# Kernel tuning notes

Measured on AMD Instinct MI355X. Metric: run time of the kernel, lower is better.

Reference implementation:

```python
import jax, jax.numpy as jnp
import numpy as np

HEAD_DIM = 128


def block_causal_mask(cu_seqlens, seq_len, dtype):
    # positions -> which packed document each token belongs to
    positions = jnp.arange(seq_len)
    seq_ids = jnp.searchsorted(cu_seqlens, positions, side='right') - 1
    same_seq = seq_ids[:, None] == seq_ids[None, :]
    causal = positions[None, :] <= positions[:, None]  # key_pos <= query_pos
    neg_inf = jnp.asarray(float('-inf'), dtype)
    return jnp.where(same_seq & causal, jnp.asarray(0.0, dtype), neg_inf)


def setup_inputs() -> dict:
    key = jax.random.key(0)
    kq, kk, kv = jax.random.split(key, 3)
    B, H, S, D = 1, 8, 4096, HEAD_DIM
    q = jax.random.normal(kq, (B, H, S, D), dtype=jnp.float32)
    k = jax.random.normal(kk, (B, H, S, D), dtype=jnp.float32)
    v = jax.random.normal(kv, (B, H, S, D), dtype=jnp.float32)
    # 4 packed documents of length 1024 each; cu_seqlens[-1] == seq_len
    cu_seqlens = jnp.array([0, 1024, 2048, 3072, 4096], dtype=jnp.int32)
    return {"q": q, "k": k, "v": v, "cu_seqlens": cu_seqlens, "max_seqlen": 1024}


def reference(q, k, v, cu_seqlens, max_seqlen):
    seq_len = q.shape[2]
    scale = 1.0 / jnp.sqrt(jnp.asarray(q.shape[-1], q.dtype))
    mask = block_causal_mask(cu_seqlens, seq_len, q.dtype)  # [S, S]
    # scores: [B, H, Sq, Sk]
    scores = jnp.einsum('bhqd,bhkd->bhqk', q, k) * scale + mask
    probs = jax.nn.softmax(scores, axis=-1)
    return jnp.einsum('bhqk,bhkd->bhqd', probs, v)
```

## Files before the change

### kernel.cpp

```cpp
#include <hip/hip_runtime.h>
#include <hip/hip_bf16.h>


#define HD 128
#define BR 64
#define BC 64

typedef __attribute__((ext_vector_type(8))) short short8;
typedef __attribute__((ext_vector_type(4))) float floatx4;

__device__ inline unsigned packbf2(float lo, float hi) {
    __hip_bfloat162 h2 = __float22bfloat162_rn(make_float2(lo, hi));
    return *reinterpret_cast<unsigned*>(&h2);
}
__device__ inline short bfs(float f) {
    __hip_bfloat16 b = __float2bfloat16(f);
    return *reinterpret_cast<short*>(&b);
}

__device__ inline void gll16(const void* g, void* l) {
    __builtin_amdgcn_global_load_lds(
        (const __attribute__((address_space(1))) unsigned int*)g,
        (__attribute__((address_space(3))) unsigned int*)l, 16, 0, 0);
}

__global__ __launch_bounds__(256) void prepack(
    const float* __restrict__ K, const float* __restrict__ V,
    unsigned short* __restrict__ wsK, unsigned short* __restrict__ wsVT,
    int S)
{
    const int tid = threadIdx.x;
    const int nKblk = (8 * S * 16) / 256;
    const int bid = blockIdx.x;
    if (bid < nKblk) {
        const int cid = bid * 256 + tid;
        const int row = cid >> 4;
        const int c   = cid & 15;
        const float* src = K + (size_t)row * HD + c * 8;
        float4 f0 = *(const float4*)src;
        float4 f1 = *(const float4*)(src + 4);
        union { uint4 q; unsigned u[4]; } w;
        w.u[0] = packbf2(f0.x, f0.y); w.u[1] = packbf2(f0.z, f0.w);
        w.u[2] = packbf2(f1.x, f1.y); w.u[3] = packbf2(f1.z, f1.w);
        *(uint4*)((char*)wsK + (size_t)row * 256 + ((c * 16) ^ ((row & 7) << 4))) = w.q;
    } else {
        const int ntile = S >> 6;
        const int b = bid - nKblk;
        const int h = b / ntile;
        const int t = b - h * ntile;
        const int d  = tid & 127;
        const int jj = tid >> 7;
        const float* vb = V + ((size_t)h * S + t * 64) * HD + d;
        char* dstrow = (char*)wsVT + ((size_t)(h * ntile + t) * HD + d) * 128;
        const int dx = (d & 7) << 4;
        #pragma unroll
        for (int u = 0; u < 4; ++u) {
            const int j  = jj * 4 + u;
            const int k0 = (j >> 2) * 32 + (j & 3) * 4;
            float v0 = vb[(size_t)(k0 +  0) * HD];
            float v1 = vb[(size_t)(k0 +  1) * HD];
            float v2 = vb[(size_t)(k0 +  2) * HD];
            float v3 = vb[(size_t)(k0 +  3) * HD];
            float v4 = vb[(size_t)(k0 + 16) * HD];
            float v5 = vb[(size_t)(k0 + 17) * HD];
            float v6 = vb[(size_t)(k0 + 18) * HD];
            float v7 = vb[(size_t)(k0 + 19) * HD];
            union { uint4 q; unsigned u4[4]; } w;
            w.u4[0] = packbf2(v0, v1); w.u4[1] = packbf2(v2, v3);
            w.u4[2] = packbf2(v4, v5); w.u4[3] = packbf2(v6, v7);
            *(uint4*)(dstrow + ((j * 16) ^ dx)) = w.q;
        }
    }
}

__global__ __launch_bounds__(256, 2) void fa_fwd(
    const float* __restrict__ Q,
    const unsigned short* __restrict__ wsK,
    const unsigned short* __restrict__ wsVT,
    const int* __restrict__ cu_seqlens, int n_cu,
    float* __restrict__ O,
    int S)
{
    __shared__ alignas(16) __hip_bfloat16 sK[2][BC * HD];
    __shared__ alignas(16) unsigned int   sVT[2][HD * 32];

    const int tid  = threadIdx.x;
    const int wave = tid >> 6;
    const int lane = tid & 63;
    const int quad = lane >> 4;
    const int l16  = lane & 15;
    const int kx   = (l16 & 7) << 4;

    const int nqb = S / BR;
    const int h   = blockIdx.x & 7;
    const int g   = (int)(blockIdx.x >> 3);
    int qb;
    if (nqb == 64) {
        if (g < 32) qb = (g >> 4) * 16 + (15 - (g & 15));
        else        qb = 32 + (((g - 32) >> 4) * 16) + (g & 15);
    } else {
        qb = nqb - 1 - g;
    }
    const int q0    = qb * BR;
    const int qw    = q0 + wave * 16;
    const int qlane = qw + l16;

    int blk_ds = 0;
    for (int i = 0; i < n_cu; ++i) {
        int c = cu_seqlens[i];
        if (c <= q0) blk_ds = c;
    }
    const int k_begin = blk_ds & ~(BC - 1);
    const int ntiles  = (q0 + BR - 1 - k_begin) / BC + 1;

    const char* gkb = (const char*)wsK + (size_t)h * S * 256;
    const char* gvb = (const char*)wsVT + (size_t)h * (S >> 6) * 16384;
    const int lo = lane * 16;
    auto stage = [&](int kt, int buf) {
        const char* gk = gkb + (size_t)kt * 256 + wave * 4096 + lo;
        const char* gv = gvb + (size_t)(kt >> 6) * 16384 + wave * 4096 + lo;
        char* lk = (char*)&sK[buf][0] + wave * 4096;
        char* lv = (char*)&sVT[buf][0] + wave * 4096;
        #pragma unroll
        for (int c = 0; c < 4; ++c) gll16(gk + c * 1024, lk + c * 1024);
        #pragma unroll
        for (int c = 0; c < 4; ++c) gll16(gv + c * 1024, lv + c * 1024);
    };

    stage(k_begin, 0);

    const size_t hoff = (size_t)h * S * HD;
    const float* Qh = Q + hoff;
    float*       Oh = O + hoff;

    int ds_lane = 0;
    for (int i = 0; i < n_cu; ++i) {
        int c = cu_seqlens[i];
        if (c <= qlane) ds_lane = c;
    }

    short8 aq[4];
    {
        const float* qp = Qh + (size_t)qlane * HD + quad * 8;
        #pragma unroll
        for (int ks = 0; ks < 4; ++ks) {
            float4 a0 = *(const float4*)(qp + ks * 32);
            float4 a1 = *(const float4*)(qp + ks * 32 + 4);
            short8 a;
            a[0] = bfs(a0.x); a[1] = bfs(a0.y); a[2] = bfs(a0.z); a[3] = bfs(a0.w);
            a[4] = bfs(a1.x); a[5] = bfs(a1.y); a[6] = bfs(a1.z); a[7] = bfs(a1.w);
            aq[ks] = a;
        }
    }

    floatx4 oacc[8];
    #pragma unroll
    for (int dt = 0; dt < 8; ++dt) oacc[dt] = (floatx4){0.f, 0.f, 0.f, 0.f};
    float m_r = -1e30f, l_r = 0.f;

    const float sl = 0.08838834764831845f * 1.4426950408889634f;

    __syncthreads();

    for (int it = 0; it < ntiles; ++it) {
        const int kt  = k_begin + it * BC;
        const int buf = it & 1;

        if (it + 1 < ntiles) stage(kt + BC, buf ^ 1);

        const char* kbase = (const char*)&sK[buf][0];
        const char* vbase = (const char*)&sVT[buf][0];

        floatx4 sc[4];
        __builtin_amdgcn_s_setprio(1);
        #pragma unroll
        for (int ct = 0; ct < 4; ++ct) {
            if (kt + ct * 16 <= qw + 15) {
                floatx4 c = (floatx4){0.f, 0.f, 0.f, 0.f};
                #pragma unroll
                for (int ks = 0; ks < 4; ++ks) {
                    short8 a = *(const short8*)(kbase + (ct * 16 + l16) * 256
                                                + (((ks * 4 + quad) << 4) ^ kx));
                    c = __builtin_amdgcn_mfma_f32_16x16x32_bf16(a, aq[ks], c, 0, 0, 0);
                }
                sc[ct] = c;
            } else {
                sc[ct] = (floatx4){-1e30f, -1e30f, -1e30f, -1e30f};
            }
        }
        __builtin_amdgcn_s_setprio(0);

        #pragma unroll
        for (int ct = 0; ct < 4; ++ct) {
            if (kt + ct * 16 <= qw + 15) {
                #pragma unroll
                for (int r = 0; r < 4; ++r) {
                    const int key = kt + ct * 16 + quad * 4 + r;
                    const bool valid = (key <= qlane) && (key >= ds_lane);
                    float s = sc[ct][r] * sl;
                    sc[ct][r] = valid ? s : -1e30f;
                }
            }
        }

        float mx0 = fmaxf(fmaxf(sc[0][0], sc[0][1]), fmaxf(sc[0][2], sc[0][3]));
        float mx1 = fmaxf(fmaxf(sc[1][0], sc[1][1]), fmaxf(sc[1][2], sc[1][3]));
        float mx2 = fmaxf(fmaxf(sc[2][0], sc[2][1]), fmaxf(sc[2][2], sc[2][3]));
        float mx3 = fmaxf(fmaxf(sc[3][0], sc[3][1]), fmaxf(sc[3][2], sc[3][3]));
        float mx  = fmaxf(fmaxf(mx0, mx1), fmaxf(mx2, mx3));
        mx = fmaxf(mx, __shfl_xor(mx, 16, 64));
        mx = fmaxf(mx, __shfl_xor(mx, 32, 64));

        const float mnew = fmaxf(m_r, mx);
        const float al   = exp2f(m_r - mnew);
        m_r = mnew;

        float s0 = 0.f, s1 = 0.f, s2 = 0.f, s3 = 0.f;
        #pragma unroll
        for (int ct = 0; ct < 4; ++ct) {
            float p0 = exp2f(sc[ct][0] - m_r);
            float p1 = exp2f(sc[ct][1] - m_r);
            float p2 = exp2f(sc[ct][2] - m_r);
            float p3 = exp2f(sc[ct][3] - m_r);
            sc[ct][0] = p0; sc[ct][1] = p1; sc[ct][2] = p2; sc[ct][3] = p3;
            s0 += p0; s1 += p1; s2 += p2; s3 += p3;
        }
        l_r = l_r * al + ((s0 + s1) + (s2 + s3));
        #pragma unroll
        for (int dt = 0; dt < 8; ++dt) {
            #pragma unroll
            for (int r = 0; r < 4; ++r)
                oacc[dt][r] *= al;
        }

        __builtin_amdgcn_s_setprio(1);
        #pragma unroll
        for (int ks = 0; ks < 2; ++ks) {
            if (kt + ks * 32 <= qw + 15) {
                union { unsigned u[4]; short8 s; } pu;
                pu.u[0] = packbf2(sc[2*ks][0],   sc[2*ks][1]);
                pu.u[1] = packbf2(sc[2*ks][2],   sc[2*ks][3]);
                pu.u[2] = packbf2(sc[2*ks+1][0], sc[2*ks+1][1]);
                pu.u[3] = packbf2(sc[2*ks+1][2], sc[2*ks+1][3]);
                #pragma unroll
                for (int dt = 0; dt < 8; ++dt) {
                    union { uint4 q; short8 s; } cv;
                    cv.q = *(const uint4*)(vbase + (dt * 16 + l16) * 128
                                           + (((ks * 4 + quad) << 4) ^ kx));
                    oacc[dt] = __builtin_amdgcn_mfma_f32_16x16x32_bf16(cv.s, pu.s, oacc[dt], 0, 0, 0);
                }
            }
        }
        __builtin_amdgcn_s_setprio(0);

        __syncthreads();
    }

    l_r += __shfl_xor(l_r, 16, 64);
    l_r += __shfl_xor(l_r, 32, 64);
    const float inv = 1.0f / l_r;
    float* op = Oh + (size_t)qlane * HD + quad * 4;
    #pragma unroll
    for (int dt = 0; dt < 8; ++dt) {
        float4 st;
        st.x = oacc[dt][0] * inv;
        st.y = oacc[dt][1] * inv;
        st.z = oacc[dt][2] * inv;
        st.w = oacc[dt][3] * inv;
        *(float4*)(op + dt * 16) = st;
    }
}

extern "C" void kernel_launch(void* const* d_in, const int* in_sizes, int n_in,
                              void* d_out, int out_size, void* d_ws, size_t ws_size,
                              hipStream_t stream) {
    const float* q = (const float*)d_in[0];
    const float* k = (const float*)d_in[1];
    const float* v = (const float*)d_in[2];
    const int* cu = (const int*)d_in[3];
    const int n_cu = in_sizes[3];
    const int H = 8;
    const int S = in_sizes[0] / (H * HD);
    float* out = (float*)d_out;

    unsigned short* wsK  = (unsigned short*)d_ws;
    unsigned short* wsVT = wsK + (size_t)H * S * HD;

    const int nKblk = (H * S * 16) / 256;
    const int nVblk = H * (S >> 6);
    prepack<<<dim3(nKblk + nVblk), dim3(256), 0, stream>>>(k, v, wsK, wsVT, S);

    dim3 grid(H * (S / BR));
    dim3 block(256);
    fa_fwd<<<grid, block, 0, stream>>>(q, wsK, wsVT, cu, n_cu, out, S);
}
```

Baseline: 139.1 us.

## Enlarge query tile to 256 rows with 8 waves each handling two 16-row chunks

Raises the query block from 64 to 256 rows and the workgroup from 256 to 512 threads. Each wave now owns 32 query rows split into two 16-row chunks, so every K fragment read from LDS feeds both chunks' MFMAs and each staged K/V tile serves four times as many queries. The V transpose in the prepack kernel now goes through shared memory with coalesced row loads instead of strided column gathers. The cost is a grid of only 128 workgroups with no causal load-balancing order, more registers per wave, and waves idling on tiles beyond their causal range while still joining every barrier.

```diff
diff --git a/kernel.cpp b/kernel.cpp
--- a/kernel.cpp
+++ b/kernel.cpp
@@ -3,7 +3,7 @@
 
 
 #define HD 128
-#define BR 64
+#define BR 256
 #define BC 64
 
 typedef __attribute__((ext_vector_type(8))) short short8;
@@ -30,7 +30,7 @@
     int S)
 {
     const int tid = threadIdx.x;
-    const int nKblk = (8 * S * 16) / 256;
+    const int nKblk = (8 * S) / 16;
     const int bid = blockIdx.x;
     if (bid < nKblk) {
         const int cid = bid * 256 + tid;
@@ -44,36 +44,52 @@
         w.u[2] = packbf2(f1.x, f1.y); w.u[3] = packbf2(f1.z, f1.w);
         *(uint4*)((char*)wsK + (size_t)row * 256 + ((c * 16) ^ ((row & 7) << 4))) = w.q;
     } else {
+        __shared__ __align__(8) unsigned short sV[HD * 68];
         const int ntile = S >> 6;
         const int b = bid - nKblk;
         const int h = b / ntile;
         const int t = b - h * ntile;
-        const int d  = tid & 127;
-        const int jj = tid >> 7;
-        const float* vb = V + ((size_t)h * S + t * 64) * HD + d;
-        char* dstrow = (char*)wsVT + ((size_t)(h * ntile + t) * HD + d) * 128;
+        const float* vb = V + ((size_t)h * S + t * 64) * HD;
+        {
+            const int rp = tid >> 3;
+            const int dc = tid & 7;
+            const int r0 = rp * 2;
+            const int d0 = dc * 16;
+            const float* p0 = vb + (size_t)r0 * HD + d0;
+            const float* p1 = p0 + HD;
+            float4 a0 = *(const float4*)(p0 + 0),  a1 = *(const float4*)(p0 + 4);
+            float4 a2 = *(const float4*)(p0 + 8),  a3 = *(const float4*)(p0 + 12);
+            float4 b0 = *(const float4*)(p1 + 0),  b1 = *(const float4*)(p1 + 4);
+            float4 b2 = *(const float4*)(p1 + 8),  b3 = *(const float4*)(p1 + 12);
+            float av[16] = {a0.x,a0.y,a0.z,a0.w, a1.x,a1.y,a1.z,a1.w,
+                            a2.x,a2.y,a2.z,a2.w, a3.x,a3.y,a3.z,a3.w};
+            float bv[16] = {b0.x,b0.y,b0.z,b0.w, b1.x,b1.y,b1.z,b1.w,
+                            b2.x,b2.y,b2.z,b2.w, b3.x,b3.y,b3.z,b3.w};
+            #pragma unroll
+            for (int i = 0; i < 16; ++i) {
+                unsigned pr = packbf2(av[i], bv[i]);
+                *(unsigned*)((char*)sV + ((size_t)(d0 + i) * 68 + r0) * 2) = pr;
+            }
+        }
+        __syncthreads();
+        const int d  = tid >> 1;
+        const int jj = tid & 1;
+        char* dstrow = (char*)wsVT + (((size_t)(h * ntile + t) * HD + d) * 128);
         const int dx = (d & 7) << 4;
+        const unsigned short* srow = sV + (size_t)d * 68;
         #pragma unroll
         for (int u = 0; u < 4; ++u) {
             const int j  = jj * 4 + u;
             const int k0 = (j >> 2) * 32 + (j & 3) * 4;
-            float v0 = vb[(size_t)(k0 +  0) * HD];
-            float v1 = vb[(size_t)(k0 +  1) * HD];
-            float v2 = vb[(size_t)(k0 +  2) * HD];
-            float v3 = vb[(size_t)(k0 +  3) * HD];
-            float v4 = vb[(size_t)(k0 + 16) * HD];
-            float v5 = vb[(size_t)(k0 + 17) * HD];
-            float v6 = vb[(size_t)(k0 + 18) * HD];
-            float v7 = vb[(size_t)(k0 + 19) * HD];
-            union { uint4 q; unsigned u4[4]; } w;
-            w.u4[0] = packbf2(v0, v1); w.u4[1] = packbf2(v2, v3);
-            w.u4[2] = packbf2(v4, v5); w.u4[3] = packbf2(v6, v7);
-            *(uint4*)(dstrow + ((j * 16) ^ dx)) = w.q;
-        }
-    }
-}
-
-__global__ __launch_bounds__(256, 2) void fa_fwd(
+            uint2 lo = *(const uint2*)(srow + k0);
+            uint2 hi = *(const uint2*)(srow + k0 + 16);
+            uint4 w = make_uint4(lo.x, lo.y, hi.x, hi.y);
+            *(uint4*)(dstrow + ((j * 16) ^ dx)) = w;
+        }
+    }
+}
+
+__global__ __launch_bounds__(512, 2) void fa_fwd(
     const float* __restrict__ Q,
     const unsigned short* __restrict__ wsK,
     const unsigned short* __restrict__ wsVT,
@@ -91,19 +107,10 @@
     const int l16  = lane & 15;
     const int kx   = (l16 & 7) << 4;
 
-    const int nqb = S / BR;
-    const int h   = blockIdx.x & 7;
-    const int g   = (int)(blockIdx.x >> 3);
-    int qb;
-    if (nqb == 64) {
-        if (g < 32) qb = (g >> 4) * 16 + (15 - (g & 15));
-        else        qb = 32 + (((g - 32) >> 4) * 16) + (g & 15);
-    } else {
-        qb = nqb - 1 - g;
-    }
-    const int q0    = qb * BR;
-    const int qw    = q0 + wave * 16;
-    const int qlane = qw + l16;
+    const int h = blockIdx.x & 7;
+    const int g = (int)(blockIdx.x >> 3);
+    const int q0  = g * BR;
+    const int qw0 = q0 + wave * 32;
 
     int blk_ds = 0;
     for (int i = 0; i < n_cu; ++i) {
@@ -115,16 +122,14 @@
 
     const char* gkb = (const char*)wsK + (size_t)h * S * 256;
     const char* gvb = (const char*)wsVT + (size_t)h * (S >> 6) * 16384;
-    const int lo = lane * 16;
+    const int lo = wave * 1024 + lane * 16;
     auto stage = [&](int kt, int buf) {
-        const char* gk = gkb + (size_t)kt * 256 + wave * 4096 + lo;
-        const char* gv = gvb + (size_t)(kt >> 6) * 16384 + wave * 4096 + lo;
-        char* lk = (char*)&sK[buf][0] + wave * 4096;
-        char* lv = (char*)&sVT[buf][0] + wave * 4096;
-        #pragma unroll
-        for (int c = 0; c < 4; ++c) gll16(gk + c * 1024, lk + c * 1024);
-        #pragma unroll
-        for (int c = 0; c < 4; ++c) gll16(gv + c * 1024, lv + c * 1024);
+        const char* gk = gkb + (size_t)kt * 256 + lo;
+        const char* gv = gvb + (size_t)(kt >> 6) * 16384 + lo;
+        char* lk = (char*)&sK[buf][0] + wave * 1024;
+        char* lv = (char*)&sVT[buf][0] + wave * 1024;
+        gll16(gk, lk);            gll16(gk + 8192, lk + 8192);
+        gll16(gv, lv);            gll16(gv + 8192, lv + 8192);
     };
 
     stage(k_begin, 0);
@@ -133,15 +138,22 @@
     const float* Qh = Q + hoff;
     float*       Oh = O + hoff;
 
-    int ds_lane = 0;
-    for (int i = 0; i < n_cu; ++i) {
-        int c = cu_seqlens[i];
-        if (c <= qlane) ds_lane = c;
-    }
-
-    short8 aq[4];
-    {
-        const float* qp = Qh + (size_t)qlane * HD + quad * 8;
+    int qlane[2], ds_l[2];
+    #pragma unroll
+    for (int c = 0; c < 2; ++c) {
+        qlane[c] = qw0 + c * 16 + l16;
+        int d = 0;
+        for (int i = 0; i < n_cu; ++i) {
+            int cc = cu_seqlens[i];
+            if (cc <= qlane[c]) d = cc;
+        }
+        ds_l[c] = d;
+    }
+
+    short8 aq[2][4];
+    #pragma unroll
+    for (int c = 0; c < 2; ++c) {
+        const float* qp = Qh + (size_t)qlane[c] * HD + quad * 8;
         #pragma unroll
         for (int ks = 0; ks < 4; ++ks) {
             float4 a0 = *(const float4*)(qp + ks * 32);
@@ -149,14 +161,17 @@
             short8 a;
             a[0] = bfs(a0.x); a[1] = bfs(a0.y); a[2] = bfs(a0.z); a[3] = bfs(a0.w);
             a[4] = bfs(a1.x); a[5] = bfs(a1.y); a[6] = bfs(a1.z); a[7] = bfs(a1.w);
-            aq[ks] = a;
-        }
-    }
-
-    floatx4 oacc[8];
+            aq[c][ks] = a;
+        }
+    }
+
+    floatx4 oacc[2][8];
     #pragma unroll
-    for (int dt = 0; dt < 8; ++dt) oacc[dt] = (floatx4){0.f, 0.f, 0.f, 0.f};
-    float m_r = -1e30f, l_r = 0.f;
+    for (int c = 0; c < 2; ++c)
+        #pragma unroll
+        for (int dt = 0; dt < 8; ++dt) oacc[c][dt] = (floatx4){0.f, 0.f, 0.f, 0.f};
+    float m_r[2] = {-1e30f, -1e30f};
+    float l_r[2] = {0.f, 0.f};
 
     const float sl = 0.08838834764831845f * 1.4426950408889634f;
 
@@ -168,106 +183,140 @@
 
         if (it + 1 < ntiles) stage(kt + BC, buf ^ 1);
 
-        const char* kbase = (const char*)&sK[buf][0];
-        const char* vbase = (const char*)&sVT[buf][0];
-
-        floatx4 sc[4];
-        __builtin_amdgcn_s_setprio(1);
-        #pragma unroll
-        for (int ct = 0; ct < 4; ++ct) {
-            if (kt + ct * 16 <= qw + 15) {
-                floatx4 c = (floatx4){0.f, 0.f, 0.f, 0.f};
+        if (kt <= qw0 + 31) {
+            const bool act0 = (kt <= qw0 + 15);
+            const char* kbase = (const char*)&sK[buf][0];
+            const char* vbase = (const char*)&sVT[buf][0];
+
+            floatx4 sc[2][4];
+            __builtin_amdgcn_s_setprio(1);
+            #pragma unroll
+            for (int ct = 0; ct < 4; ++ct) {
+                const int kc = kt + ct * 16;
+                if (kc <= qw0 + 31) {
+                    short8 a[4];
+                    #pragma unroll
+                    for (int ks = 0; ks < 4; ++ks)
+                        a[ks] = *(const short8*)(kbase + (ct * 16 + l16) * 256
+                                                 + (((ks * 4 + quad) << 4) ^ kx));
+                    floatx4 c1 = (floatx4){0.f, 0.f, 0.f, 0.f};
+                    #pragma unroll
+                    for (int ks = 0; ks < 4; ++ks)
+                        c1 = __builtin_amdgcn_mfma_f32_16x16x32_bf16(a[ks], aq[1][ks], c1, 0, 0, 0);
+                    sc[1][ct] = c1;
+                    if (kc <= qw0 + 15) {
+                        floatx4 c0 = (floatx4){0.f, 0.f, 0.f, 0.f};
+                        #pragma unroll
+                        for (int ks = 0; ks < 4; ++ks)
+                            c0 = __builtin_amdgcn_mfma_f32_16x16x32_bf16(a[ks], aq[0][ks], c0, 0, 0, 0);
+                        sc[0][ct] = c0;
+                    } else {
+                        sc[0][ct] = (floatx4){-1e30f, -1e30f, -1e30f, -1e30f};
+                    }
+                } else {
+                    sc[0][ct] = (floatx4){-1e30f, -1e30f, -1e30f, -1e30f};
+                    sc[1][ct] = (floatx4){-1e30f, -1e30f, -1e30f, -1e30f};
+                }
+            }
+            __builtin_amdgcn_s_setprio(0);
+
+            #pragma unroll
+            for (int c = 0; c < 2; ++c) {
+                if (c == 0 && !act0) continue;
                 #pragma unroll
-                for (int ks = 0; ks < 4; ++ks) {
-                    short8 a = *(const short8*)(kbase + (ct * 16 + l16) * 256
-                                                + (((ks * 4 + quad) << 4) ^ kx));
-                    c = __builtin_amdgcn_mfma_f32_16x16x32_bf16(a, aq[ks], c, 0, 0, 0);
-                }
-                sc[ct] = c;
-            } else {
-                sc[ct] = (floatx4){-1e30f, -1e30f, -1e30f, -1e30f};
+                for (int ct = 0; ct < 4; ++ct) {
+                    if (kt + ct * 16 <= qw0 + c * 16 + 15) {
+                        #pragma unroll
+                        for (int r = 0; r < 4; ++r) {
+                            const int key = kt + ct * 16 + quad * 4 + r;
+                            const bool valid = (key <= qlane[c]) && (key >= ds_l[c]);
+                            float s = sc[c][ct][r] * sl;
+                            sc[c][ct][r] = valid ? s : -1e30f;
+                        }
+                    }
+                }
+                float mx0 = fmaxf(fmaxf(sc[c][0][0], sc[c][0][1]), fmaxf(sc[c][0][2], sc[c][0][3]));
+                float mx1 = fmaxf(fmaxf(sc[c][1][0], sc[c][1][1]), fmaxf(sc[c][1][2], sc[c][1][3]));
+                float mx2 = fmaxf(fmaxf(sc[c][2][0], sc[c][2][1]), fmaxf(sc[c][2][2], sc[c][2][3]));
+                float mx3 = fmaxf(fmaxf(sc[c][3][0], sc[c][3][1]), fmaxf(sc[c][3][2], sc[c][3][3]));
+                float mx  = fmaxf(fmaxf(mx0, mx1), fmaxf(mx2, mx3));
+                mx = fmaxf(mx, __shfl_xor(mx, 16, 64));
+                mx = fmaxf(mx, __shfl_xor(mx, 32, 64));
+
+                const float mnew = fmaxf(m_r[c], mx);
+                const float al   = exp2f(m_r[c] - mnew);
+                m_r[c] = mnew;
+
+                float s0 = 0.f, s1 = 0.f, s2 = 0.f, s3 = 0.f;
+                #pragma unroll
+                for (int ct = 0; ct < 4; ++ct) {
+                    float p0 = exp2f(sc[c][ct][0] - m_r[c]);
+                    float p1 = exp2f(sc[c][ct][1] - m_r[c]);
+                    float p2 = exp2f(sc[c][ct][2] - m_r[c]);
+                    float p3 = exp2f(sc[c][ct][3] - m_r[c]);
+                    sc[c][ct][0] = p0; sc[c][ct][1] = p1;
+                    sc[c][ct][2] = p2; sc[c][ct][3] = p3;
+                    s0 += p0; s1 += p1; s2 += p2; s3 += p3;
+                }
+                l_r[c] = l_r[c] * al + ((s0 + s1) + (s2 + s3));
+                #pragma unroll
+                for (int dt = 0; dt < 8; ++dt) {
+                    #pragma unroll
+                    for (int r = 0; r < 4; ++r)
+                        oacc[c][dt][r] *= al;
+                }
             }
-        }
-        __builtin_amdgcn_s_setprio(0);
-
-        #pragma unroll
-        for (int ct = 0; ct < 4; ++ct) {
-            if (kt + ct * 16 <= qw + 15) {
-                #pragma unroll
-                for (int r = 0; r < 4; ++r) {
-                    const int key = kt + ct * 16 + quad * 4 + r;
-                    const bool valid = (key <= qlane) && (key >= ds_lane);
-                    float s = sc[ct][r] * sl;
-                    sc[ct][r] = valid ? s : -1e30f;
+
+            __builtin_amdgcn_s_setprio(1);
+            #pragma unroll
+            for (int ks = 0; ks < 2; ++ks) {
+                const int kh = kt + ks * 32;
+                if (kh <= qw0 + 31) {
+                    union { unsigned u[4]; short8 s; } pu1, pu0;
+                    pu1.u[0] = packbf2(sc[1][2*ks][0],   sc[1][2*ks][1]);
+                    pu1.u[1] = packbf2(sc[1][2*ks][2],   sc[1][2*ks][3]);
+                    pu1.u[2] = packbf2(sc[1][2*ks+1][0], sc[1][2*ks+1][1]);
+                    pu1.u[3] = packbf2(sc[1][2*ks+1][2], sc[1][2*ks+1][3]);
+                    const bool p0a = (kh <= qw0 + 15);
+                    if (p0a) {
+                        pu0.u[0] = packbf2(sc[0][2*ks][0],   sc[0][2*ks][1]);
+                        pu0.u[1] = packbf2(sc[0][2*ks][2],   sc[0][2*ks][3]);
+                        pu0.u[2] = packbf2(sc[0][2*ks+1][0], sc[0][2*ks+1][1]);
+                        pu0.u[3] = packbf2(sc[0][2*ks+1][2], sc[0][2*ks+1][3]);
+                    }
+                    #pragma unroll
+                    for (int dt = 0; dt < 8; ++dt) {
+                        union { uint4 q; short8 s; } cv;
+                        cv.q = *(const uint4*)(vbase + (dt * 16 + l16) * 128
+                                               + (((ks * 4 + quad) << 4) ^ kx));
+                        oacc[1][dt] = __builtin_amdgcn_mfma_f32_16x16x32_bf16(cv.s, pu1.s, oacc[1][dt], 0, 0, 0);
+                        if (p0a)
+                            oacc[0][dt] = __builtin_amdgcn_mfma_f32_16x16x32_bf16(cv.s, pu0.s, oacc[0][dt], 0, 0, 0);
+                    }
                 }
             }
-        }
-
-        float mx0 = fmaxf(fmaxf(sc[0][0], sc[0][1]), fmaxf(sc[0][2], sc[0][3]));
-        float mx1 = fmaxf(fmaxf(sc[1][0], sc[1][1]), fmaxf(sc[1][2], sc[1][3]));
-        float mx2 = fmaxf(fmaxf(sc[2][0], sc[2][1]), fmaxf(sc[2][2], sc[2][3]));
-        float mx3 = fmaxf(fmaxf(sc[3][0], sc[3][1]), fmaxf(sc[3][2], sc[3][3]));
-        float mx  = fmaxf(fmaxf(mx0, mx1), fmaxf(mx2, mx3));
-        mx = fmaxf(mx, __shfl_xor(mx, 16, 64));
-        mx = fmaxf(mx, __shfl_xor(mx, 32, 64));
-
-        const float mnew = fmaxf(m_r, mx);
-        const float al   = exp2f(m_r - mnew);
-        m_r = mnew;
-
-        float s0 = 0.f, s1 = 0.f, s2 = 0.f, s3 = 0.f;
-        #pragma unroll
-        for (int ct = 0; ct < 4; ++ct) {
-            float p0 = exp2f(sc[ct][0] - m_r);
-            float p1 = exp2f(sc[ct][1] - m_r);
-            float p2 = exp2f(sc[ct][2] - m_r);
-            float p3 = exp2f(sc[ct][3] - m_r);
-            sc[ct][0] = p0; sc[ct][1] = p1; sc[ct][2] = p2; sc[ct][3] = p3;
-            s0 += p0; s1 += p1; s2 += p2; s3 += p3;
-        }
-        l_r = l_r * al + ((s0 + s1) + (s2 + s3));
+            __builtin_amdgcn_s_setprio(0);
+        }
+
+        __syncthreads();
+    }
+
+    #pragma unroll
+    for (int c = 0; c < 2; ++c) {
+        float l = l_r[c];
+        l += __shfl_xor(l, 16, 64);
+        l += __shfl_xor(l, 32, 64);
+        const float inv = 1.0f / l;
+        float* op = Oh + (size_t)qlane[c] * HD + quad * 4;
         #pragma unroll
         for (int dt = 0; dt < 8; ++dt) {
-            #pragma unroll
-            for (int r = 0; r < 4; ++r)
-                oacc[dt][r] *= al;
-        }
-
-        __builtin_amdgcn_s_setprio(1);
-        #pragma unroll
-        for (int ks = 0; ks < 2; ++ks) {
-            if (kt + ks * 32 <= qw + 15) {
-                union { unsigned u[4]; short8 s; } pu;
-                pu.u[0] = packbf2(sc[2*ks][0],   sc[2*ks][1]);
-                pu.u[1] = packbf2(sc[2*ks][2],   sc[2*ks][3]);
-                pu.u[2] = packbf2(sc[2*ks+1][0], sc[2*ks+1][1]);
-                pu.u[3] = packbf2(sc[2*ks+1][2], sc[2*ks+1][3]);
-                #pragma unroll
-                for (int dt = 0; dt < 8; ++dt) {
-                    union { uint4 q; short8 s; } cv;
-                    cv.q = *(const uint4*)(vbase + (dt * 16 + l16) * 128
-                                           + (((ks * 4 + quad) << 4) ^ kx));
-                    oacc[dt] = __builtin_amdgcn_mfma_f32_16x16x32_bf16(cv.s, pu.s, oacc[dt], 0, 0, 0);
-                }
-            }
-        }
-        __builtin_amdgcn_s_setprio(0);
-
-        __syncthreads();
-    }
-
-    l_r += __shfl_xor(l_r, 16, 64);
-    l_r += __shfl_xor(l_r, 32, 64);
-    const float inv = 1.0f / l_r;
-    float* op = Oh + (size_t)qlane * HD + quad * 4;
-    #pragma unroll
-    for (int dt = 0; dt < 8; ++dt) {
-        float4 st;
-        st.x = oacc[dt][0] * inv;
-        st.y = oacc[dt][1] * inv;
-        st.z = oacc[dt][2] * inv;
-        st.w = oacc[dt][3] * inv;
-        *(float4*)(op + dt * 16) = st;
+            float4 st;
+            st.x = oacc[c][dt][0] * inv;
+            st.y = oacc[c][dt][1] * inv;
+            st.z = oacc[c][dt][2] * inv;
+            st.w = oacc[c][dt][3] * inv;
+            *(float4*)(op + dt * 16) = st;
+        }
     }
 }
 
@@ -286,11 +335,11 @@
     unsigned short* wsK  = (unsigned short*)d_ws;
     unsigned short* wsVT = wsK + (size_t)H * S * HD;
 
-    const int nKblk = (H * S * 16) / 256;
+    const int nKblk = (H * S) / 16;
     const int nVblk = H * (S >> 6);
     prepack<<<dim3(nKblk + nVblk), dim3(256), 0, stream>>>(k, v, wsK, wsVT, S);
 
     dim3 grid(H * (S / BR));
-    dim3 block(256);
+    dim3 block(512);
     fa_fwd<<<grid, block, 0, stream>>>(q, wsK, wsVT, cu, n_cu, out, S);
 }
```

New measurement: 170.0 us. 1.22x slower.

## Split long KV chains across two blocks and transpose V via LDS in prepack

Applied to the files above, without the earlier changes.

Query blocks whose KV tile chain is longer than MAXCHAIN are split into two halves, handled by separate workgroups. Each half writes unnormalized partial output plus max and sum statistics to workspace, and the last block to finish (found with an atomic counter) merges them. This shortens the critical path so the grid balances better, at the cost of extra partial writes, a memset and a merge pass. Separately, prepack now transposes V through shared memory with coalesced float4 loads instead of strided scalar reads. The split path is only taken if the workspace is large enough.

```diff
diff --git a/kernel.cpp b/kernel.cpp
--- a/kernel.cpp
+++ b/kernel.cpp
@@ -5,6 +5,7 @@
 #define HD 128
 #define BR 64
 #define BC 64
+#define MAXCHAIN 8
 
 typedef __attribute__((ext_vector_type(8))) short short8;
 typedef __attribute__((ext_vector_type(4))) float floatx4;
@@ -30,7 +31,7 @@
     int S)
 {
     const int tid = threadIdx.x;
-    const int nKblk = (8 * S * 16) / 256;
+    const int nKblk = (8 * S) / 16;
     const int bid = blockIdx.x;
     if (bid < nKblk) {
         const int cid = bid * 256 + tid;
@@ -44,31 +45,47 @@
         w.u[2] = packbf2(f1.x, f1.y); w.u[3] = packbf2(f1.z, f1.w);
         *(uint4*)((char*)wsK + (size_t)row * 256 + ((c * 16) ^ ((row & 7) << 4))) = w.q;
     } else {
+        __shared__ __align__(8) unsigned short sV[HD * 68];
         const int ntile = S >> 6;
         const int b = bid - nKblk;
         const int h = b / ntile;
         const int t = b - h * ntile;
-        const int d  = tid & 127;
-        const int jj = tid >> 7;
-        const float* vb = V + ((size_t)h * S + t * 64) * HD + d;
-        char* dstrow = (char*)wsVT + ((size_t)(h * ntile + t) * HD + d) * 128;
+        const float* vb = V + ((size_t)h * S + t * 64) * HD;
+        {
+            const int rp = tid >> 3;
+            const int dc = tid & 7;
+            const int r0 = rp * 2;
+            const int d0 = dc * 16;
+            const float* p0 = vb + (size_t)r0 * HD + d0;
+            const float* p1 = p0 + HD;
+            float4 a0 = *(const float4*)(p0 + 0),  a1 = *(const float4*)(p0 + 4);
+            float4 a2 = *(const float4*)(p0 + 8),  a3 = *(const float4*)(p0 + 12);
+            float4 b0 = *(const float4*)(p1 + 0),  b1 = *(const float4*)(p1 + 4);
+            float4 b2 = *(const float4*)(p1 + 8),  b3 = *(const float4*)(p1 + 12);
+            float av[16] = {a0.x,a0.y,a0.z,a0.w, a1.x,a1.y,a1.z,a1.w,
+                            a2.x,a2.y,a2.z,a2.w, a3.x,a3.y,a3.z,a3.w};
+            float bv[16] = {b0.x,b0.y,b0.z,b0.w, b1.x,b1.y,b1.z,b1.w,
+                            b2.x,b2.y,b2.z,b2.w, b3.x,b3.y,b3.z,b3.w};
+            #pragma unroll
+            for (int i = 0; i < 16; ++i) {
+                unsigned pr = packbf2(av[i], bv[i]);
+                *(unsigned*)((char*)sV + ((size_t)(d0 + i) * 68 + r0) * 2) = pr;
+            }
+        }
+        __syncthreads();
+        const int d  = tid >> 1;
+        const int jj = tid & 1;
+        char* dstrow = (char*)wsVT + (((size_t)(h * ntile + t) * HD + d) * 128);
         const int dx = (d & 7) << 4;
+        const unsigned short* srow = sV + (size_t)d * 68;
         #pragma unroll
         for (int u = 0; u < 4; ++u) {
             const int j  = jj * 4 + u;
             const int k0 = (j >> 2) * 32 + (j & 3) * 4;
-            float v0 = vb[(size_t)(k0 +  0) * HD];
-            float v1 = vb[(size_t)(k0 +  1) * HD];
-            float v2 = vb[(size_t)(k0 +  2) * HD];
-            float v3 = vb[(size_t)(k0 +  3) * HD];
-            float v4 = vb[(size_t)(k0 + 16) * HD];
-            float v5 = vb[(size_t)(k0 + 17) * HD];
-            float v6 = vb[(size_t)(k0 + 18) * HD];
-            float v7 = vb[(size_t)(k0 + 19) * HD];
-            union { uint4 q; unsigned u4[4]; } w;
-            w.u4[0] = packbf2(v0, v1); w.u4[1] = packbf2(v2, v3);
-            w.u4[2] = packbf2(v4, v5); w.u4[3] = packbf2(v6, v7);
-            *(uint4*)(dstrow + ((j * 16) ^ dx)) = w.q;
+            uint2 lo = *(const uint2*)(srow + k0);
+            uint2 hi = *(const uint2*)(srow + k0 + 16);
+            uint4 w = make_uint4(lo.x, lo.y, hi.x, hi.y);
+            *(uint4*)(dstrow + ((j * 16) ^ dx)) = w;
         }
     }
 }
@@ -79,10 +96,12 @@
     const unsigned short* __restrict__ wsVT,
     const int* __restrict__ cu_seqlens, int n_cu,
     float* __restrict__ O,
-    int S)
+    int S, int split_en,
+    unsigned* __restrict__ cnt, float* __restrict__ part)
 {
     __shared__ alignas(16) __hip_bfloat16 sK[2][BC * HD];
     __shared__ alignas(16) unsigned int   sVT[2][HD * 32];
+    __shared__ int rank_sh;
 
     const int tid  = threadIdx.x;
     const int wave = tid >> 6;
@@ -93,13 +112,17 @@
 
     const int nqb = S / BR;
     const int h   = blockIdx.x & 7;
-    const int g   = (int)(blockIdx.x >> 3);
-    int qb;
-    if (nqb == 64) {
-        if (g < 32) qb = (g >> 4) * 16 + (15 - (g & 15));
-        else        qb = 32 + (((g - 32) >> 4) * 16) + (g & 15);
+    int g = (int)(blockIdx.x >> 3);
+    int qb, piece;
+    if (split_en) {
+        qb    = nqb - 1 - (g >> 1);
+        piece = g & 1;
     } else {
-        qb = nqb - 1 - g;
+        piece = 0;
+        if (nqb == 64) {
+            if (g < 32) qb = (g >> 4) * 16 + (15 - (g & 15));
+            else        qb = 32 + (((g - 32) >> 4) * 16) + (g & 15);
+        } else qb = nqb - 1 - g;
     }
     const int q0    = qb * BR;
     const int qw    = q0 + wave * 16;
@@ -111,7 +134,12 @@
         if (c <= q0) blk_ds = c;
     }
     const int k_begin = blk_ds & ~(BC - 1);
-    const int ntiles  = (q0 + BR - 1 - k_begin) / BC + 1;
+    const int n = (q0 + BR - 1 - k_begin) / BC + 1;
+
+    const bool split = split_en && (n > MAXCHAIN);
+    if (!split && piece) return;
+    const int it0 = (split && piece)  ? n / 2 : 0;
+    const int it1 = (split && !piece) ? n / 2 : n;
 
     const char* gkb = (const char*)wsK + (size_t)h * S * 256;
     const char* gvb = (const char*)wsVT + (size_t)h * (S >> 6) * 16384;
@@ -127,7 +155,7 @@
         for (int c = 0; c < 4; ++c) gll16(gv + c * 1024, lv + c * 1024);
     };
 
-    stage(k_begin, 0);
+    stage(k_begin + it0 * BC, 0);
 
     const size_t hoff = (size_t)h * S * HD;
     const float* Qh = Q + hoff;
@@ -162,11 +190,11 @@
 
     __syncthreads();
 
-    for (int it = 0; it < ntiles; ++it) {
+    for (int it = it0; it < it1; ++it) {
         const int kt  = k_begin + it * BC;
-        const int buf = it & 1;
-
-        if (it + 1 < ntiles) stage(kt + BC, buf ^ 1);
+        const int buf = (it - it0) & 1;
+
+        if (it + 1 < it1) stage(k_begin + (it + 1) * BC, buf ^ 1);
 
         const char* kbase = (const char*)&sK[buf][0];
         const char* vbase = (const char*)&sVT[buf][0];
@@ -258,16 +286,68 @@
 
     l_r += __shfl_xor(l_r, 16, 64);
     l_r += __shfl_xor(l_r, 32, 64);
-    const float inv = 1.0f / l_r;
-    float* op = Oh + (size_t)qlane * HD + quad * 4;
+
+    if (!split) {
+        const float inv = 1.0f / l_r;
+        float* op = Oh + (size_t)qlane * HD + quad * 4;
+        #pragma unroll
+        for (int dt = 0; dt < 8; ++dt) {
+            float4 st;
+            st.x = oacc[dt][0] * inv;
+            st.y = oacc[dt][1] * inv;
+            st.z = oacc[dt][2] * inv;
+            st.w = oacc[dt][3] * inv;
+            *(float4*)(op + dt * 16) = st;
+        }
+        return;
+    }
+
+    const int slot = h * nqb + qb;
+    float* pb = part + (size_t)slot * 16640 + piece * 8192;
+    const int qlocal = wave * 16 + l16;
+    {
+        float* orow = pb + (size_t)qlocal * 128 + quad * 4;
+        #pragma unroll
+        for (int dt = 0; dt < 8; ++dt) {
+            float4 st;
+            st.x = oacc[dt][0]; st.y = oacc[dt][1];
+            st.z = oacc[dt][2]; st.w = oacc[dt][3];
+            *(float4*)(orow + dt * 16) = st;
+        }
+        float* mlb = part + (size_t)slot * 16640 + 16384;
+        if (quad == 0) {
+            mlb[piece * 128 + qlocal]      = m_r;
+            mlb[piece * 128 + 64 + qlocal] = l_r;
+        }
+    }
+    __threadfence();
+    __syncthreads();
+    if (tid == 0) rank_sh = (int)atomicAdd(&cnt[slot], 1u);
+    __syncthreads();
+    if (rank_sh != 1) return;
+
+    __threadfence();
+    const float* O1  = part + (size_t)slot * 16640;
+    const float* O2  = O1 + 8192;
+    const float* mlb = O1 + 16384;
     #pragma unroll
-    for (int dt = 0; dt < 8; ++dt) {
-        float4 st;
-        st.x = oacc[dt][0] * inv;
-        st.y = oacc[dt][1] * inv;
-        st.z = oacc[dt][2] * inv;
-        st.w = oacc[dt][3] * inv;
-        *(float4*)(op + dt * 16) = st;
+    for (int kk = 0; kk < 8; ++kk) {
+        const int fidx = tid + kk * 256;
+        const int row  = fidx >> 5;
+        const int c4   = fidx & 31;
+        const float m1 = mlb[row],       l1 = mlb[64 + row];
+        const float m2 = mlb[128 + row], l2 = mlb[192 + row];
+        const float M  = fmaxf(m1, m2);
+        const float w1 = exp2f(m1 - M), w2 = exp2f(m2 - M);
+        const float inv = 1.0f / (w1 * l1 + w2 * l2);
+        float4 a = *(const float4*)(O1 + (size_t)fidx * 4);
+        float4 b = *(const float4*)(O2 + (size_t)fidx * 4);
+        float4 o;
+        o.x = (w1 * a.x + w2 * b.x) * inv;
+        o.y = (w1 * a.y + w2 * b.y) * inv;
+        o.z = (w1 * a.z + w2 * b.z) * inv;
+        o.w = (w1 * a.w + w2 * b.w) * inv;
+        *(float4*)(Oh + (size_t)(q0 + row) * HD + c4 * 4) = o;
     }
 }
 
@@ -283,14 +363,24 @@
     const int S = in_sizes[0] / (H * HD);
     float* out = (float*)d_out;
 
+    const int nqb = S / BR;
     unsigned short* wsK  = (unsigned short*)d_ws;
     unsigned short* wsVT = wsK + (size_t)H * S * HD;
-
-    const int nKblk = (H * S * 16) / 256;
+    const size_t kvbytes = (size_t)2 * H * S * HD * 2;
+    const size_t cntbytes = ((size_t)H * nqb * 4 + 255) & ~(size_t)255;
+    unsigned* cnt = (unsigned*)((char*)d_ws + kvbytes);
+    float* part = (float*)((char*)d_ws + kvbytes + cntbytes);
+    const size_t need = kvbytes + cntbytes + (size_t)H * nqb * 66560;
+    const int split_en = (ws_size >= need) ? 1 : 0;
+
+    if (split_en) hipMemsetAsync(cnt, 0, (size_t)H * nqb * 4, stream);
+
+    const int nKblk = (H * S) / 16;
     const int nVblk = H * (S >> 6);
     prepack<<<dim3(nKblk + nVblk), dim3(256), 0, stream>>>(k, v, wsK, wsVT, S);
 
-    dim3 grid(H * (S / BR));
+    dim3 grid(H * nqb * (split_en ? 2 : 1));
     dim3 block(256);
-    fa_fwd<<<grid, block, 0, stream>>>(q, wsK, wsVT, cu, n_cu, out, S);
-}
+    fa_fwd<<<grid, block, 0, stream>>>(q, wsK, wsVT, cu, n_cu, out, S,
+                                       split_en, cnt, part);
+}
```

After: 245.0 us. 1.76x slower.

## Split key tiles across two wave groups and transpose V through LDS in prepack

Applied to the files above, without the earlier changes.

The attention kernel now runs 512 threads per block. Two groups of four waves each take half of every 64-key tile and keep their own online softmax state, and the two partial outputs are merged through LDS at the end. The prepack transpose of V now goes through shared memory with coalesced float4 loads instead of strided scalar loads, and V blocks are scheduled first. The query-block ordering heuristic is dropped as well. This targets low per-block parallelism and slow strided V reads, at the cost of an extra merge step and the loss of the longest-first scheduling order.

```diff
diff --git a/kernel.cpp b/kernel.cpp
--- a/kernel.cpp
+++ b/kernel.cpp
@@ -30,10 +30,52 @@
     int S)
 {
     const int tid = threadIdx.x;
-    const int nKblk = (8 * S * 16) / 256;
+    const int nVblk = 8 * (S >> 6);
     const int bid = blockIdx.x;
-    if (bid < nKblk) {
-        const int cid = bid * 256 + tid;
+    if (bid < nVblk) {
+        __shared__ __align__(8) unsigned short sV[HD * 68];
+        const int ntile = S >> 6;
+        const int h = bid / ntile;
+        const int t = bid - h * ntile;
+        const float* vb = V + ((size_t)h * S + t * 64) * HD;
+        {
+            const int rp = tid >> 3;
+            const int dc = tid & 7;
+            const int r0 = rp * 2;
+            const int d0 = dc * 16;
+            const float* p0 = vb + (size_t)r0 * HD + d0;
+            const float* p1 = p0 + HD;
+            float4 a0 = *(const float4*)(p0 + 0),  a1 = *(const float4*)(p0 + 4);
+            float4 a2 = *(const float4*)(p0 + 8),  a3 = *(const float4*)(p0 + 12);
+            float4 b0 = *(const float4*)(p1 + 0),  b1 = *(const float4*)(p1 + 4);
+            float4 b2 = *(const float4*)(p1 + 8),  b3 = *(const float4*)(p1 + 12);
+            float av[16] = {a0.x,a0.y,a0.z,a0.w, a1.x,a1.y,a1.z,a1.w,
+                            a2.x,a2.y,a2.z,a2.w, a3.x,a3.y,a3.z,a3.w};
+            float bv[16] = {b0.x,b0.y,b0.z,b0.w, b1.x,b1.y,b1.z,b1.w,
+                            b2.x,b2.y,b2.z,b2.w, b3.x,b3.y,b3.z,b3.w};
+            #pragma unroll
+            for (int i = 0; i < 16; ++i) {
+                unsigned pr = packbf2(av[i], bv[i]);
+                *(unsigned*)((char*)sV + ((size_t)(d0 + i) * 68 + r0) * 2) = pr;
+            }
+        }
+        __syncthreads();
+        const int d  = tid >> 1;
+        const int jj = tid & 1;
+        char* dstrow = (char*)wsVT + (((size_t)(h * ntile + t) * HD + d) * 128);
+        const int dx = (d & 7) << 4;
+        const unsigned short* srow = sV + (size_t)d * 68;
+        #pragma unroll
+        for (int u = 0; u < 4; ++u) {
+            const int j  = jj * 4 + u;
+            const int k0 = (j >> 2) * 32 + (j & 3) * 4;
+            uint2 lo = *(const uint2*)(srow + k0);
+            uint2 hi = *(const uint2*)(srow + k0 + 16);
+            uint4 w = make_uint4(lo.x, lo.y, hi.x, hi.y);
+            *(uint4*)(dstrow + ((j * 16) ^ dx)) = w;
+        }
+    } else {
+        const int cid = (bid - nVblk) * 256 + tid;
         const int row = cid >> 4;
         const int c   = cid & 15;
         const float* src = K + (size_t)row * HD + c * 8;
@@ -43,37 +85,10 @@
         w.u[0] = packbf2(f0.x, f0.y); w.u[1] = packbf2(f0.z, f0.w);
         w.u[2] = packbf2(f1.x, f1.y); w.u[3] = packbf2(f1.z, f1.w);
         *(uint4*)((char*)wsK + (size_t)row * 256 + ((c * 16) ^ ((row & 7) << 4))) = w.q;
-    } else {
-        const int ntile = S >> 6;
-        const int b = bid - nKblk;
-        const int h = b / ntile;
-        const int t = b - h * ntile;
-        const int d  = tid & 127;
-        const int jj = tid >> 7;
-        const float* vb = V + ((size_t)h * S + t * 64) * HD + d;
-        char* dstrow = (char*)wsVT + ((size_t)(h * ntile + t) * HD + d) * 128;
-        const int dx = (d & 7) << 4;
-        #pragma unroll
-        for (int u = 0; u < 4; ++u) {
-            const int j  = jj * 4 + u;
-            const int k0 = (j >> 2) * 32 + (j & 3) * 4;
-            float v0 = vb[(size_t)(k0 +  0) * HD];
-            float v1 = vb[(size_t)(k0 +  1) * HD];
-            float v2 = vb[(size_t)(k0 +  2) * HD];
-            float v3 = vb[(size_t)(k0 +  3) * HD];
-            float v4 = vb[(size_t)(k0 + 16) * HD];
-            float v5 = vb[(size_t)(k0 + 17) * HD];
-            float v6 = vb[(size_t)(k0 + 18) * HD];
-            float v7 = vb[(size_t)(k0 + 19) * HD];
-            union { uint4 q; unsigned u4[4]; } w;
-            w.u4[0] = packbf2(v0, v1); w.u4[1] = packbf2(v2, v3);
-            w.u4[2] = packbf2(v4, v5); w.u4[3] = packbf2(v6, v7);
-            *(uint4*)(dstrow + ((j * 16) ^ dx)) = w.q;
-        }
-    }
-}
-
-__global__ __launch_bounds__(256, 2) void fa_fwd(
+    }
+}
+
+__global__ __launch_bounds__(512, 4) void fa_fwd(
     const float* __restrict__ Q,
     const unsigned short* __restrict__ wsK,
     const unsigned short* __restrict__ wsVT,
@@ -86,6 +101,8 @@
 
     const int tid  = threadIdx.x;
     const int wave = tid >> 6;
+    const int gp   = wave >> 2;
+    const int wsub = wave & 3;
     const int lane = tid & 63;
     const int quad = lane >> 4;
     const int l16  = lane & 15;
@@ -94,15 +111,9 @@
     const int nqb = S / BR;
     const int h   = blockIdx.x & 7;
     const int g   = (int)(blockIdx.x >> 3);
-    int qb;
-    if (nqb == 64) {
-        if (g < 32) qb = (g >> 4) * 16 + (15 - (g & 15));
-        else        qb = 32 + (((g - 32) >> 4) * 16) + (g & 15);
-    } else {
-        qb = nqb - 1 - g;
-    }
+    const int qb = (nqb == 64) ? g : (nqb - 1 - g);
     const int q0    = qb * BR;
-    const int qw    = q0 + wave * 16;
+    const int qw    = q0 + wsub * 16;
     const int qlane = qw + l16;
 
     int blk_ds = 0;
@@ -115,16 +126,20 @@
 
     const char* gkb = (const char*)wsK + (size_t)h * S * 256;
     const char* gvb = (const char*)wsVT + (size_t)h * (S >> 6) * 16384;
-    const int lo = lane * 16;
+    const int wofs = (wave & 3) * 4096;
+    const int lo = wofs + lane * 16;
     auto stage = [&](int kt, int buf) {
-        const char* gk = gkb + (size_t)kt * 256 + wave * 4096 + lo;
-        const char* gv = gvb + (size_t)(kt >> 6) * 16384 + wave * 4096 + lo;
-        char* lk = (char*)&sK[buf][0] + wave * 4096;
-        char* lv = (char*)&sVT[buf][0] + wave * 4096;
-        #pragma unroll
-        for (int c = 0; c < 4; ++c) gll16(gk + c * 1024, lk + c * 1024);
-        #pragma unroll
-        for (int c = 0; c < 4; ++c) gll16(gv + c * 1024, lv + c * 1024);
+        if (gp == 0) {
+            const char* gk = gkb + (size_t)kt * 256 + lo;
+            char* lk = (char*)&sK[buf][0] + wofs;
+            #pragma unroll
+            for (int c = 0; c < 4; ++c) gll16(gk + c * 1024, lk + c * 1024);
+        } else {
+            const char* gv = gvb + (size_t)(kt >> 6) * 16384 + lo;
+            char* lv = (char*)&sVT[buf][0] + wofs;
+            #pragma unroll
+            for (int c = 0; c < 4; ++c) gll16(gv + c * 1024, lv + c * 1024);
+        }
     };
 
     stage(k_begin, 0);
@@ -168,106 +183,131 @@
 
         if (it + 1 < ntiles) stage(kt + BC, buf ^ 1);
 
-        const char* kbase = (const char*)&sK[buf][0];
-        const char* vbase = (const char*)&sVT[buf][0];
-
-        floatx4 sc[4];
-        __builtin_amdgcn_s_setprio(1);
-        #pragma unroll
-        for (int ct = 0; ct < 4; ++ct) {
-            if (kt + ct * 16 <= qw + 15) {
-                floatx4 c = (floatx4){0.f, 0.f, 0.f, 0.f};
-                #pragma unroll
-                for (int ks = 0; ks < 4; ++ks) {
-                    short8 a = *(const short8*)(kbase + (ct * 16 + l16) * 256
-                                                + (((ks * 4 + quad) << 4) ^ kx));
-                    c = __builtin_amdgcn_mfma_f32_16x16x32_bf16(a, aq[ks], c, 0, 0, 0);
+        if (kt + gp * 32 <= qw + 15) {
+            const char* kbase = (const char*)&sK[buf][0];
+            const char* vbase = (const char*)&sVT[buf][0];
+
+            floatx4 sc[2];
+            __builtin_amdgcn_s_setprio(1);
+            #pragma unroll
+            for (int ctl = 0; ctl < 2; ++ctl) {
+                const int ct = 2 * gp + ctl;
+                if (kt + ct * 16 <= qw + 15) {
+                    floatx4 c = (floatx4){0.f, 0.f, 0.f, 0.f};
+                    #pragma unroll
+                    for (int ks = 0; ks < 4; ++ks) {
+                        short8 a = *(const short8*)(kbase + (ct * 16 + l16) * 256
+                                                    + (((ks * 4 + quad) << 4) ^ kx));
+                        c = __builtin_amdgcn_mfma_f32_16x16x32_bf16(a, aq[ks], c, 0, 0, 0);
+                    }
+                    sc[ctl] = c;
+                } else {
+                    sc[ctl] = (floatx4){-1e30f, -1e30f, -1e30f, -1e30f};
                 }
-                sc[ct] = c;
-            } else {
-                sc[ct] = (floatx4){-1e30f, -1e30f, -1e30f, -1e30f};
-            }
-        }
-        __builtin_amdgcn_s_setprio(0);
-
-        #pragma unroll
-        for (int ct = 0; ct < 4; ++ct) {
-            if (kt + ct * 16 <= qw + 15) {
+            }
+            __builtin_amdgcn_s_setprio(0);
+
+            #pragma unroll
+            for (int ctl = 0; ctl < 2; ++ctl) {
+                if (kt + (2 * gp + ctl) * 16 <= qw + 15) {
+                    #pragma unroll
+                    for (int r = 0; r < 4; ++r) {
+                        const int key = kt + (2 * gp + ctl) * 16 + quad * 4 + r;
+                        const bool valid = (key <= qlane) && (key >= ds_lane);
+                        float s = sc[ctl][r] * sl;
+                        sc[ctl][r] = valid ? s : -1e30f;
+                    }
+                }
+            }
+
+            float mx = fmaxf(fmaxf(fmaxf(sc[0][0], sc[0][1]), fmaxf(sc[0][2], sc[0][3])),
+                             fmaxf(fmaxf(sc[1][0], sc[1][1]), fmaxf(sc[1][2], sc[1][3])));
+            mx = fmaxf(mx, __shfl_xor(mx, 16, 64));
+            mx = fmaxf(mx, __shfl_xor(mx, 32, 64));
+
+            const float mnew = fmaxf(m_r, mx);
+            const float al   = exp2f(m_r - mnew);
+            const float live = (mnew > -1e29f) ? 1.f : 0.f;
+            m_r = mnew;
+
+            float ssum = 0.f;
+            #pragma unroll
+            for (int ctl = 0; ctl < 2; ++ctl) {
                 #pragma unroll
                 for (int r = 0; r < 4; ++r) {
-                    const int key = kt + ct * 16 + quad * 4 + r;
-                    const bool valid = (key <= qlane) && (key >= ds_lane);
-                    float s = sc[ct][r] * sl;
-                    sc[ct][r] = valid ? s : -1e30f;
+                    float p = exp2f(sc[ctl][r] - m_r) * live;
+                    sc[ctl][r] = p;
+                    ssum += p;
                 }
             }
-        }
-
-        float mx0 = fmaxf(fmaxf(sc[0][0], sc[0][1]), fmaxf(sc[0][2], sc[0][3]));
-        float mx1 = fmaxf(fmaxf(sc[1][0], sc[1][1]), fmaxf(sc[1][2], sc[1][3]));
-        float mx2 = fmaxf(fmaxf(sc[2][0], sc[2][1]), fmaxf(sc[2][2], sc[2][3]));
-        float mx3 = fmaxf(fmaxf(sc[3][0], sc[3][1]), fmaxf(sc[3][2], sc[3][3]));
-        float mx  = fmaxf(fmaxf(mx0, mx1), fmaxf(mx2, mx3));
-        mx = fmaxf(mx, __shfl_xor(mx, 16, 64));
-        mx = fmaxf(mx, __shfl_xor(mx, 32, 64));
-
-        const float mnew = fmaxf(m_r, mx);
-        const float al   = exp2f(m_r - mnew);
-        m_r = mnew;
-
-        float s0 = 0.f, s1 = 0.f, s2 = 0.f, s3 = 0.f;
-        #pragma unroll
-        for (int ct = 0; ct < 4; ++ct) {
-            float p0 = exp2f(sc[ct][0] - m_r);
-            float p1 = exp2f(sc[ct][1] - m_r);
-            float p2 = exp2f(sc[ct][2] - m_r);
-            float p3 = exp2f(sc[ct][3] - m_r);
-            sc[ct][0] = p0; sc[ct][1] = p1; sc[ct][2] = p2; sc[ct][3] = p3;
-            s0 += p0; s1 += p1; s2 += p2; s3 += p3;
-        }
-        l_r = l_r * al + ((s0 + s1) + (s2 + s3));
+            l_r = l_r * al + ssum;
+            #pragma unroll
+            for (int dt = 0; dt < 8; ++dt) {
+                #pragma unroll
+                for (int r = 0; r < 4; ++r)
+                    oacc[dt][r] *= al;
+            }
+
+            union { unsigned u[4]; short8 s; } pu;
+            pu.u[0] = packbf2(sc[0][0], sc[0][1]);
+            pu.u[1] = packbf2(sc[0][2], sc[0][3]);
+            pu.u[2] = packbf2(sc[1][0], sc[1][1]);
+            pu.u[3] = packbf2(sc[1][2], sc[1][3]);
+            __builtin_amdgcn_s_setprio(1);
+            #pragma unroll
+            for (int dt = 0; dt < 8; ++dt) {
+                union { uint4 q; short8 s; } cv;
+                cv.q = *(const uint4*)(vbase + (dt * 16 + l16) * 128
+                                       + (((gp * 4 + quad) << 4) ^ kx));
+                oacc[dt] = __builtin_amdgcn_mfma_f32_16x16x32_bf16(cv.s, pu.s, oacc[dt], 0, 0, 0);
+            }
+            __builtin_amdgcn_s_setprio(0);
+        }
+
+        __syncthreads();
+    }
+
+    l_r += __shfl_xor(l_r, 16, 64);
+    l_r += __shfl_xor(l_r, 32, 64);
+
+    float* obuf = (float*)&sK[0][0];
+    float* lbuf = (float*)&sVT[0][0];
+    if (gp == 1) {
+        float* ob = obuf + wsub * 2048;
         #pragma unroll
         for (int dt = 0; dt < 8; ++dt) {
-            #pragma unroll
-            for (int r = 0; r < 4; ++r)
-                oacc[dt][r] *= al;
-        }
-
-        __builtin_amdgcn_s_setprio(1);
+            const int sw = (dt ^ (lane & 7)) << 2;
+            float4 st;
+            st.x = oacc[dt][0]; st.y = oacc[dt][1];
+            st.z = oacc[dt][2]; st.w = oacc[dt][3];
+            *(float4*)(ob + lane * 32 + sw) = st;
+        }
+        if (quad == 0) {
+            lbuf[wsub * 128 + l16]      = m_r;
+            lbuf[wsub * 128 + 64 + l16] = l_r;
+        }
+    }
+    __syncthreads();
+    if (gp == 0) {
+        const float m2 = lbuf[wsub * 128 + l16];
+        const float l2 = lbuf[wsub * 128 + 64 + l16];
+        const float M  = fmaxf(m_r, m2);
+        const float w1 = exp2f(m_r - M);
+        const float w2 = exp2f(m2 - M);
+        const float inv = 1.0f / (w1 * l_r + w2 * l2);
+        const float* ob = obuf + wsub * 2048;
+        float* op = Oh + (size_t)qlane * HD + quad * 4;
         #pragma unroll
-        for (int ks = 0; ks < 2; ++ks) {
-            if (kt + ks * 32 <= qw + 15) {
-                union { unsigned u[4]; short8 s; } pu;
-                pu.u[0] = packbf2(sc[2*ks][0],   sc[2*ks][1]);
-                pu.u[1] = packbf2(sc[2*ks][2],   sc[2*ks][3]);
-                pu.u[2] = packbf2(sc[2*ks+1][0], sc[2*ks+1][1]);
-                pu.u[3] = packbf2(sc[2*ks+1][2], sc[2*ks+1][3]);
-                #pragma unroll
-                for (int dt = 0; dt < 8; ++dt) {
-                    union { uint4 q; short8 s; } cv;
-                    cv.q = *(const uint4*)(vbase + (dt * 16 + l16) * 128
-                                           + (((ks * 4 + quad) << 4) ^ kx));
-                    oacc[dt] = __builtin_amdgcn_mfma_f32_16x16x32_bf16(cv.s, pu.s, oacc[dt], 0, 0, 0);
-                }
-            }
-        }
-        __builtin_amdgcn_s_setprio(0);
-
-        __syncthreads();
-    }
-
-    l_r += __shfl_xor(l_r, 16, 64);
-    l_r += __shfl_xor(l_r, 32, 64);
-    const float inv = 1.0f / l_r;
-    float* op = Oh + (size_t)qlane * HD + quad * 4;
-    #pragma unroll
-    for (int dt = 0; dt < 8; ++dt) {
-        float4 st;
-        st.x = oacc[dt][0] * inv;
-        st.y = oacc[dt][1] * inv;
-        st.z = oacc[dt][2] * inv;
-        st.w = oacc[dt][3] * inv;
-        *(float4*)(op + dt * 16) = st;
+        for (int dt = 0; dt < 8; ++dt) {
+            const int sw = (dt ^ (lane & 7)) << 2;
+            float4 o2 = *(const float4*)(ob + lane * 32 + sw);
+            float4 st;
+            st.x = (w1 * oacc[dt][0] + w2 * o2.x) * inv;
+            st.y = (w1 * oacc[dt][1] + w2 * o2.y) * inv;
+            st.z = (w1 * oacc[dt][2] + w2 * o2.z) * inv;
+            st.w = (w1 * oacc[dt][3] + w2 * o2.w) * inv;
+            *(float4*)(op + dt * 16) = st;
+        }
     }
 }
 
@@ -283,14 +323,15 @@
     const int S = in_sizes[0] / (H * HD);
     float* out = (float*)d_out;
 
+    const int nqb = S / BR;
     unsigned short* wsK  = (unsigned short*)d_ws;
     unsigned short* wsVT = wsK + (size_t)H * S * HD;
 
-    const int nKblk = (H * S * 16) / 256;
     const int nVblk = H * (S >> 6);
-    prepack<<<dim3(nKblk + nVblk), dim3(256), 0, stream>>>(k, v, wsK, wsVT, S);
-
-    dim3 grid(H * (S / BR));
-    dim3 block(256);
+    const int nKblk = (H * S) / 16;
+    prepack<<<dim3(nVblk + nKblk), dim3(256), 0, stream>>>(k, v, wsK, wsVT, S);
+
+    dim3 grid(H * nqb);
+    dim3 block(512);
     fa_fwd<<<grid, block, 0, stream>>>(q, wsK, wsVT, cu, n_cu, out, S);
 }
```

Result: faster. 135.4 us (-2.6%).
